# Kernel optimization log

Measured on AMD Instinct MI355X. Metric: run time of the kernel, lower is better.

The kernel has to match this reference:

```python
import jax, jax.numpy as jnp
import numpy as np

N = 1_000_000
C = 128
NBINS = 15


def setup_inputs() -> dict:
    key = jax.random.key(0)
    k1, k2 = jax.random.split(key)
    logits = jax.random.normal(k1, (N, C), dtype=jnp.float32)
    labels = jax.random.randint(k2, (N,), 0, C, dtype=jnp.int64)
    return {"logits": logits, "labels": labels}


def reference(logits, labels):
    n = logits.shape[0]
    probs = jax.nn.softmax(logits, axis=1)
    confidences = jnp.max(probs, axis=1)                      # [N]
    predictions = jnp.argmax(probs, axis=1)                   # [N]
    accuracies = (predictions == labels).astype(jnp.float32)  # [N]

    # Equal-count (adaptive) bin edges: interp(linspace(0,N,nbins+1), arange(N), sort(conf))
    sorted_conf = jnp.sort(confidences)
    q = jnp.linspace(0.0, float(n), NBINS + 1)
    edges = jnp.interp(q, jnp.arange(n, dtype=jnp.float32), sorted_conf)  # [NBINS+1]

    # Bin i covers (edges[i], edges[i+1]] to match conf.gt(lower) & conf.le(upper).
    idx = jnp.searchsorted(edges[1:-1], confidences, side="left")  # [N] in [0, NBINS-1]
    valid = (confidences > edges[0]) & (confidences <= edges[-1])
    idx = jnp.where(valid, idx, NBINS)  # dump out-of-range into extra segment

    cnt = jax.ops.segment_sum(jnp.ones_like(confidences), idx, num_segments=NBINS + 1)[:NBINS]
    csum = jax.ops.segment_sum(confidences, idx, num_segments=NBINS + 1)[:NBINS]
    asum = jax.ops.segment_sum(accuracies, idx, num_segments=NBINS + 1)[:NBINS]

    prop = cnt / jnp.float32(n)
    safe = jnp.maximum(cnt, 1.0)
    gap = jnp.abs(csum / safe - asum / safe)
    ece = jnp.sum(jnp.where(cnt > 0, gap * prop, 0.0))
    return ece.reshape(1)
```

## Files before the change

kernel.cpp:

```cpp
#include <hip/hip_runtime.h>
#include <hip/hip_bf16.h>
#include <cstdint>

#define NROWS 1000000
#define NCLS  128
#define NBINS 15

#define FBASE 0x3B000000u
#define NB    73728
#define SCAN_T 1024
#define PER   (NB / SCAN_T)

#define OFF_CONF   0u
#define OFF_ACC    4000000u
#define OFF_HIST   5000000u
#define OFF_SUB    5294912u
#define OFF_BINS   5417792u
#define OFF_DONE   5418152u
#define OFF_TGTB   5418168u
#define OFF_TGTL   5418288u
#define OFF_EDGES  5418408u
#define ZERO_BYTES (OFF_TGTB - OFF_HIST)

__device__ __forceinline__ float swz_max(float m, const int off)
{
    switch (off) {
    case 1: return fmaxf(m, __uint_as_float(__builtin_amdgcn_ds_swizzle(__float_as_uint(m), 0x041F)));
    case 2: return fmaxf(m, __uint_as_float(__builtin_amdgcn_ds_swizzle(__float_as_uint(m), 0x081F)));
    case 4: return fmaxf(m, __uint_as_float(__builtin_amdgcn_ds_swizzle(__float_as_uint(m), 0x101F)));
    default:return fmaxf(m, __uint_as_float(__builtin_amdgcn_ds_swizzle(__float_as_uint(m), 0x201F)));
    }
}
__device__ __forceinline__ float swz_add(float s, const int off)
{
    switch (off) {
    case 1: return s + __uint_as_float(__builtin_amdgcn_ds_swizzle(__float_as_uint(s), 0x041F));
    case 2: return s + __uint_as_float(__builtin_amdgcn_ds_swizzle(__float_as_uint(s), 0x081F));
    case 4: return s + __uint_as_float(__builtin_amdgcn_ds_swizzle(__float_as_uint(s), 0x101F));
    default:return s + __uint_as_float(__builtin_amdgcn_ds_swizzle(__float_as_uint(s), 0x201F));
    }
}

__global__ __launch_bounds__(256) void k_row(const float* __restrict__ logits,
                                             const int* __restrict__ labels,
                                             float* __restrict__ conf,
                                             unsigned char* __restrict__ acc,
                                             unsigned int* __restrict__ histT)
{
    const int lane = threadIdx.x & 63;
    const int wv   = threadIdx.x >> 6;
    const int g    = lane >> 4;
    const int l16  = lane & 15;
    const int wbase = blockIdx.x * 32 + wv * 8;
    const float4* lg4 = reinterpret_cast<const float4*>(logits);

#pragma unroll
    for (int half = 0; half < 2; half++) {
        const int row = wbase + half * 4 + g;
        const float4 v0 = lg4[row * 32 + l16];
        const float4 v1 = lg4[row * 32 + 16 + l16];
        const int lab = labels[row];

        float m = fmaxf(fmaxf(fmaxf(v0.x, v0.y), fmaxf(v0.z, v0.w)),
                        fmaxf(fmaxf(v1.x, v1.y), fmaxf(v1.z, v1.w)));
        m = swz_max(m, 1); m = swz_max(m, 2); m = swz_max(m, 4); m = swz_max(m, 8);

        float s = __expf(v0.x) + __expf(v0.y) + __expf(v0.z) + __expf(v0.w)
                + __expf(v1.x) + __expf(v1.y) + __expf(v1.z) + __expf(v1.w);
        s = swz_add(s, 1); s = swz_add(s, 2); s = swz_add(s, 4); s = swz_add(s, 8);

        const float c = __expf(m) / s;

        const bool hiHalf = (lab & 64) != 0;
        const float cx = hiHalf ? v1.x : v0.x;
        const float cy = hiHalf ? v1.y : v0.y;
        const float cz = hiHalf ? v1.z : v0.z;
        const float cw = hiHalf ? v1.w : v0.w;
        const int e = lab & 3;
        const float cand = (e == 0) ? cx : (e == 1) ? cy : (e == 2) ? cz : cw;
        const bool hit = (((lab >> 2) & 15) == l16) && (cand == m);
        const unsigned long long bal = __ballot(hit);

        if (l16 == 15) {
            conf[row] = c;
            acc[row]  = ((bal >> (lane & 48)) & 0xFFFFull) ? 1u : 0u;
            int ub = (int)(__float_as_uint(c) - FBASE);
            int b  = ub >> 10;
            b = b < 0 ? 0 : (b >= NB ? NB - 1 : b);
            atomicAdd(&histT[(b % PER) * 1024 + b / PER], 1u);
        }
    }
}

__device__ __forceinline__ unsigned int rank_of(int s)
{
    if (s == 0)  return 0u;
    if (s == 29) return (unsigned int)(NROWS - 1);
    int i = (s + 1) >> 1;
    unsigned int k = (unsigned int)((long long)i * NROWS / 15);
    return k + ((s & 1) ? 0u : 1u);
}

__global__ __launch_bounds__(SCAN_T) void k_scan(const unsigned int* __restrict__ histT,
                                                 int* __restrict__ tgtb,
                                                 int* __restrict__ tgtl)
{
    __shared__ unsigned int v[SCAN_T];
    const int t = threadIdx.x;
    unsigned int s = 0;
    for (int j = 0; j < PER; j++) s += histT[j * 1024 + t];
    v[t] = s;
    __syncthreads();
    for (int off = 1; off < SCAN_T; off <<= 1) {
        unsigned int x = (t >= off) ? v[t - off] : 0u;
        __syncthreads();
        v[t] += x;
        __syncthreads();
    }
    const unsigned int run0 = v[t] - s;
    for (int s2 = 0; s2 < 30; s2++) {
        unsigned int r = rank_of(s2);
        if (r >= run0 && r < run0 + s) {
            unsigned int run = run0;
            for (int j = 0; j < PER; j++) {
                unsigned int c = histT[j * 1024 + t];
                if (r < run + c) { tgtb[s2] = t * PER + j; tgtl[s2] = (int)(r - run); break; }
                run += c;
            }
        }
    }
}

__global__ __launch_bounds__(256) void k_subhist(const float* __restrict__ conf,
                                                 const int* __restrict__ tgtb,
                                                 const int* __restrict__ tgtl,
                                                 unsigned int* __restrict__ sub,
                                                 float* __restrict__ edges,
                                                 unsigned int* __restrict__ done)
{
    __shared__ int tb[30];
    if (threadIdx.x < 30) tb[threadIdx.x] = tgtb[threadIdx.x];
    __syncthreads();
    const int stride = gridDim.x * blockDim.x;
    for (int i = blockIdx.x * blockDim.x + threadIdx.x; i < NROWS / 4; i += stride) {
        float4 c4 = reinterpret_cast<const float4*>(conf)[i];
        float cv[4] = {c4.x, c4.y, c4.z, c4.w};
#pragma unroll
        for (int e = 0; e < 4; e++) {
            int ub = (int)(__float_as_uint(cv[e]) - FBASE);
            int b  = ub >> 10;
            b = b < 0 ? 0 : (b >= NB ? NB - 1 : b);
            int lo = ub & 1023;
            int match = -1;
#pragma unroll
            for (int s = 0; s < 30; s++) match = (b == tb[s]) ? s : match;
            if (match >= 0) atomicAdd(&sub[match * 1024 + lo], 1u);
        }
    }

    __syncthreads();
    __shared__ unsigned int isLast;
    if (threadIdx.x == 0) {
        __threadfence();
        isLast = (atomicAdd(done, 1u) == gridDim.x - 1) ? 1u : 0u;
    }
    __syncthreads();
    if (!isLast) return;
    __threadfence();

    __shared__ float val[32];
    const int k = threadIdx.x & 31;
    for (int slot = threadIdx.x >> 5; slot < 30; slot += 8) {
        const unsigned int local = (unsigned int)tgtl[slot];
        unsigned int cs[32];
        unsigned int csum = 0;
        const unsigned int* q = sub + slot * 1024 + k * 32;
#pragma unroll
        for (int j = 0; j < 32; j++) { cs[j] = q[j]; csum += cs[j]; }
        unsigned int incl = csum;
#pragma unroll
        for (int off = 1; off < 32; off <<= 1) {
            unsigned int x = __shfl_up(incl, off);
            if (k >= off) incl += x;
        }
        const unsigned int excl = incl - csum;
        if (local >= excl && local < excl + csum) {
            unsigned int run = excl;
            int subidx = 0;
#pragma unroll
            for (int j = 0; j < 32; j++) {
                if (local >= run && local < run + cs[j]) subidx = k * 32 + j;
                run += cs[j];
            }
            unsigned int bits = FBASE + ((unsigned int)tb[slot] << 10) + (unsigned int)subidx;
            val[slot] = __uint_as_float(bits);
        }
    }
    __syncthreads();
    if (threadIdx.x == 0) {
        edges[0]  = val[0];
        edges[15] = val[29];
        for (int i = 1; i <= 14; i++) {
            double q = (double)i * (double)NROWS / 15.0;
            long long kk = (long long)i * NROWS / 15;
            double f = q - (double)kk;
            edges[i] = (float)((1.0 - f) * (double)val[2 * i - 1] + f * (double)val[2 * i]);
        }
    }
}

__global__ __launch_bounds__(256) void k_bin(const float* __restrict__ conf,
                                             const unsigned char* __restrict__ acc,
                                             const float* __restrict__ edges,
                                             double* __restrict__ bins,
                                             unsigned int* __restrict__ done,
                                             float* __restrict__ out)
{
    __shared__ float se[16];
    __shared__ float lc[4][16], ls[4][16], la[4][16];
    const int w = threadIdx.x >> 6;
    if (threadIdx.x < 16) se[threadIdx.x] = edges[threadIdx.x];
    if (threadIdx.x < 64) {
        int a = threadIdx.x >> 4, b = threadIdx.x & 15;
        lc[a][b] = 0.f; ls[a][b] = 0.f; la[a][b] = 0.f;
    }
    __syncthreads();
    const int stride = gridDim.x * blockDim.x;
    for (int i = blockIdx.x * blockDim.x + threadIdx.x; i < NROWS / 4; i += stride) {
        float4 c4 = reinterpret_cast<const float4*>(conf)[i];
        uchar4 a4 = reinterpret_cast<const uchar4*>(acc)[i];
        float cv[4] = {c4.x, c4.y, c4.z, c4.w};
        unsigned char av[4] = {a4.x, a4.y, a4.z, a4.w};
#pragma unroll
        for (int e = 0; e < 4; e++) {
            float v = cv[e];
            if (v > se[0] && v <= se[15]) {
                int idx = 0;
#pragma unroll
                for (int j = 1; j <= 14; j++) idx += (se[j] < v) ? 1 : 0;
                atomicAdd(&lc[w][idx], 1.0f);
                atomicAdd(&ls[w][idx], v);
                atomicAdd(&la[w][idx], (float)av[e]);
            }
        }
    }
    __syncthreads();
    if (threadIdx.x < 15) {
        int t = threadIdx.x;
        atomicAdd(&bins[t],      (double)(lc[0][t] + lc[1][t] + lc[2][t] + lc[3][t]));
        atomicAdd(&bins[15 + t], (double)(ls[0][t] + ls[1][t] + ls[2][t] + ls[3][t]));
        atomicAdd(&bins[30 + t], (double)(la[0][t] + la[1][t] + la[2][t] + la[3][t]));
    }

    __syncthreads();
    __shared__ unsigned int isLast;
    if (threadIdx.x == 0) {
        __threadfence();
        isLast = (atomicAdd(done, 1u) == gridDim.x - 1) ? 1u : 0u;
    }
    __syncthreads();
    if (isLast && threadIdx.x == 0) {
        __threadfence();
        double ece = 0.0;
        for (int b = 0; b < NBINS; b++) {
            double cnt = bins[b];
            if (cnt > 0.0) {
                double safe = cnt < 1.0 ? 1.0 : cnt;
                double gap  = fabs(bins[15 + b] / safe - bins[30 + b] / safe);
                ece += gap * (cnt / (double)NROWS);
            }
        }
        out[0] = (float)ece;
    }
}

extern "C" void kernel_launch(void* const* d_in, const int* in_sizes, int n_in,
                              void* d_out, int out_size, void* d_ws, size_t ws_size,
                              hipStream_t stream)
{
    const float* logits = (const float*)d_in[0];
    const int*   labels = (const int*)d_in[1];
    char* ws = (char*)d_ws;

    float*         conf  = (float*)(ws + OFF_CONF);
    unsigned char* acc   = (unsigned char*)(ws + OFF_ACC);
    unsigned int*  histT = (unsigned int*)(ws + OFF_HIST);
    unsigned int*  sub   = (unsigned int*)(ws + OFF_SUB);
    double*        bins  = (double*)(ws + OFF_BINS);
    unsigned int*  done  = (unsigned int*)(ws + OFF_DONE);
    int*           tgtb  = (int*)(ws + OFF_TGTB);
    int*           tgtl  = (int*)(ws + OFF_TGTL);
    float*         edges = (float*)(ws + OFF_EDGES);

    hipMemsetAsync(ws + OFF_HIST, 0, ZERO_BYTES, stream);

    k_row<<<NROWS / 32, 256, 0, stream>>>(logits, labels, conf, acc, histT);
    k_scan<<<1, SCAN_T, 0, stream>>>(histT, tgtb, tgtl);
    k_subhist<<<1024, 256, 0, stream>>>(conf, tgtb, tgtl, sub, edges, done);
    k_bin<<<1024, 256, 0, stream>>>(conf, acc, edges, bins, done + 1, (float*)d_out);
}
```

Measured before the change: 257.3 us.

## Split last-block reductions into separate kernels and spread LDS atomics across slices

Replaces the last-block-done atomic pattern in the subhist and bin kernels with dedicated single-block kernels (k_edges, k_final) that read per-block partials. The bin kernel now accumulates into 64 padded LDS slices instead of 4 per-wave copies, which cuts LDS atomic contention, and writes float partials instead of doing global double atomics. The subhist kernel swaps its 30-way linear match for a 5-step binary search over the sorted target buckets, with duplicate buckets resolved in k_edges. The cost is two extra kernel launches and a larger LDS footprint per block in k_bin.

Result: faster. 215.9 us (-16.1%).

```diff
diff --git a/kernel.cpp b/kernel.cpp
--- a/kernel.cpp
+++ b/kernel.cpp
@@ -15,12 +15,11 @@
 #define OFF_ACC    4000000u
 #define OFF_HIST   5000000u
 #define OFF_SUB    5294912u
-#define OFF_BINS   5417792u
-#define OFF_DONE   5418152u
-#define OFF_TGTB   5418168u
-#define OFF_TGTL   5418288u
-#define OFF_EDGES  5418408u
-#define ZERO_BYTES (OFF_TGTB - OFF_HIST)
+#define OFF_PART   5417792u
+#define OFF_TGTB   5614400u
+#define OFF_TGTL   5614520u
+#define OFF_EDGES  5614640u
+#define ZERO_BYTES (OFF_PART - OFF_HIST)
 
 __device__ __forceinline__ float swz_max(float m, const int off)
 {
@@ -133,13 +132,10 @@
 
 __global__ __launch_bounds__(256) void k_subhist(const float* __restrict__ conf,
                                                  const int* __restrict__ tgtb,
-                                                 const int* __restrict__ tgtl,
-                                                 unsigned int* __restrict__ sub,
-                                                 float* __restrict__ edges,
-                                                 unsigned int* __restrict__ done)
-{
-    __shared__ int tb[30];
-    if (threadIdx.x < 30) tb[threadIdx.x] = tgtb[threadIdx.x];
+                                                 unsigned int* __restrict__ sub)
+{
+    __shared__ int tb[32];
+    if (threadIdx.x < 32) tb[threadIdx.x] = (threadIdx.x < 30) ? tgtb[threadIdx.x] : 0x7FFFFFFF;
     __syncthreads();
     const int stride = gridDim.x * blockDim.x;
     for (int i = blockIdx.x * blockDim.x + threadIdx.x; i < NROWS / 4; i += stride) {
@@ -150,33 +146,41 @@
             int ub = (int)(__float_as_uint(cv[e]) - FBASE);
             int b  = ub >> 10;
             b = b < 0 ? 0 : (b >= NB ? NB - 1 : b);
-            int lo = ub & 1023;
-            int match = -1;
-#pragma unroll
-            for (int s = 0; s < 30; s++) match = (b == tb[s]) ? s : match;
-            if (match >= 0) atomicAdd(&sub[match * 1024 + lo], 1u);
-        }
-    }
-
-    __syncthreads();
-    __shared__ unsigned int isLast;
-    if (threadIdx.x == 0) {
-        __threadfence();
-        isLast = (atomicAdd(done, 1u) == gridDim.x - 1) ? 1u : 0u;
-    }
-    __syncthreads();
-    if (!isLast) return;
-    __threadfence();
-
+            int lo10 = ub & 1023;
+            int lo = (tb[15] < b) ? 16 : 0;
+            lo += (tb[lo + 7] < b) ? 8 : 0;
+            lo += (tb[lo + 3] < b) ? 4 : 0;
+            lo += (tb[lo + 1] < b) ? 2 : 0;
+            lo += (tb[lo]     < b) ? 1 : 0;
+            if (tb[lo] == b) atomicAdd(&sub[lo * 1024 + lo10], 1u);
+        }
+    }
+}
+
+__global__ __launch_bounds__(1024) void k_edges(const unsigned int* __restrict__ sub,
+                        const int* __restrict__ tgtb,
+                        const int* __restrict__ tgtl,
+                        float* __restrict__ edges)
+{
     __shared__ float val[32];
+    __shared__ int tb[30], rep[30];
+    if (threadIdx.x < 30) tb[threadIdx.x] = tgtb[threadIdx.x];
+    __syncthreads();
+    if (threadIdx.x < 30) {
+        int r = 0;
+        while (tb[r] != tb[threadIdx.x]) r++;
+        rep[threadIdx.x] = r;
+    }
+    __syncthreads();
+    const int g = threadIdx.x >> 5;
     const int k = threadIdx.x & 31;
-    for (int slot = threadIdx.x >> 5; slot < 30; slot += 8) {
-        const unsigned int local = (unsigned int)tgtl[slot];
+    if (g < 30) {
+        const unsigned int local = (unsigned int)tgtl[g];
         unsigned int cs[32];
         unsigned int csum = 0;
-        const unsigned int* q = sub + slot * 1024 + k * 32;
-#pragma unroll
-        for (int j = 0; j < 32; j++) { cs[j] = q[j]; csum += cs[j]; }
+        const unsigned int* p = sub + rep[g] * 1024 + k * 32;
+#pragma unroll
+        for (int j = 0; j < 32; j++) { cs[j] = p[j]; csum += cs[j]; }
         unsigned int incl = csum;
 #pragma unroll
         for (int off = 1; off < 32; off <<= 1) {
@@ -192,8 +196,8 @@
                 if (local >= run && local < run + cs[j]) subidx = k * 32 + j;
                 run += cs[j];
             }
-            unsigned int bits = FBASE + ((unsigned int)tb[slot] << 10) + (unsigned int)subidx;
-            val[slot] = __uint_as_float(bits);
+            unsigned int bits = FBASE + ((unsigned int)tb[g] << 10) + (unsigned int)subidx;
+            val[g] = __uint_as_float(bits);
         }
     }
     __syncthreads();
@@ -212,19 +216,15 @@
 __global__ __launch_bounds__(256) void k_bin(const float* __restrict__ conf,
                                              const unsigned char* __restrict__ acc,
                                              const float* __restrict__ edges,
-                                             double* __restrict__ bins,
-                                             unsigned int* __restrict__ done,
-                                             float* __restrict__ out)
+                                             float* __restrict__ partial)
 {
     __shared__ float se[16];
-    __shared__ float lc[4][16], ls[4][16], la[4][16];
-    const int w = threadIdx.x >> 6;
+    __shared__ float sl[3][64 * 17];
     if (threadIdx.x < 16) se[threadIdx.x] = edges[threadIdx.x];
-    if (threadIdx.x < 64) {
-        int a = threadIdx.x >> 4, b = threadIdx.x & 15;
-        lc[a][b] = 0.f; ls[a][b] = 0.f; la[a][b] = 0.f;
-    }
-    __syncthreads();
+    for (int i = threadIdx.x; i < 3 * 64 * 17; i += 256) (&sl[0][0])[i] = 0.f;
+    __syncthreads();
+
+    const int slice = threadIdx.x & 63;
     const int stride = gridDim.x * blockDim.x;
     for (int i = blockIdx.x * blockDim.x + threadIdx.x; i < NROWS / 4; i += stride) {
         float4 c4 = reinterpret_cast<const float4*>(conf)[i];
@@ -238,35 +238,45 @@
                 int idx = 0;
 #pragma unroll
                 for (int j = 1; j <= 14; j++) idx += (se[j] < v) ? 1 : 0;
-                atomicAdd(&lc[w][idx], 1.0f);
-                atomicAdd(&ls[w][idx], v);
-                atomicAdd(&la[w][idx], (float)av[e]);
+                atomicAdd(&sl[0][slice * 17 + idx], 1.0f);
+                atomicAdd(&sl[1][slice * 17 + idx], v);
+                atomicAdd(&sl[2][slice * 17 + idx], (float)av[e]);
             }
         }
     }
     __syncthreads();
-    if (threadIdx.x < 15) {
-        int t = threadIdx.x;
-        atomicAdd(&bins[t],      (double)(lc[0][t] + lc[1][t] + lc[2][t] + lc[3][t]));
-        atomicAdd(&bins[15 + t], (double)(ls[0][t] + ls[1][t] + ls[2][t] + ls[3][t]));
-        atomicAdd(&bins[30 + t], (double)(la[0][t] + la[1][t] + la[2][t] + la[3][t]));
-    }
-
-    __syncthreads();
-    __shared__ unsigned int isLast;
+    if (threadIdx.x < 48) {
+        const int a = threadIdx.x >> 4, b = threadIdx.x & 15;
+        float sum = 0.f;
+        for (int s = 0; s < 64; s++) sum += sl[a][s * 17 + b];
+        partial[(a * 16 + b) * 1024 + blockIdx.x] = sum;
+    }
+}
+
+__global__ __launch_bounds__(1024) void k_final(const float* __restrict__ partial,
+                                                float* __restrict__ out)
+{
+    __shared__ double tot[48];
+    const int w    = threadIdx.x >> 6;
+    const int lane = threadIdx.x & 63;
+#pragma unroll
+    for (int c = 0; c < 3; c++) {
+        const int j = w * 3 + c;
+        double s = 0.0;
+#pragma unroll
+        for (int i = 0; i < 16; i++) s += (double)partial[j * 1024 + i * 64 + lane];
+#pragma unroll
+        for (int d = 1; d < 64; d <<= 1) s += __shfl_xor(s, d);
+        if (lane == 0) tot[j] = s;
+    }
+    __syncthreads();
     if (threadIdx.x == 0) {
-        __threadfence();
-        isLast = (atomicAdd(done, 1u) == gridDim.x - 1) ? 1u : 0u;
-    }
-    __syncthreads();
-    if (isLast && threadIdx.x == 0) {
-        __threadfence();
         double ece = 0.0;
         for (int b = 0; b < NBINS; b++) {
-            double cnt = bins[b];
+            double cnt = tot[b];
             if (cnt > 0.0) {
                 double safe = cnt < 1.0 ? 1.0 : cnt;
-                double gap  = fabs(bins[15 + b] / safe - bins[30 + b] / safe);
+                double gap  = fabs(tot[16 + b] / safe - tot[32 + b] / safe);
                 ece += gap * (cnt / (double)NROWS);
             }
         }
@@ -286,8 +296,7 @@
     unsigned char* acc   = (unsigned char*)(ws + OFF_ACC);
     unsigned int*  histT = (unsigned int*)(ws + OFF_HIST);
     unsigned int*  sub   = (unsigned int*)(ws + OFF_SUB);
-    double*        bins  = (double*)(ws + OFF_BINS);
-    unsigned int*  done  = (unsigned int*)(ws + OFF_DONE);
+    float*         part  = (float*)(ws + OFF_PART);
     int*           tgtb  = (int*)(ws + OFF_TGTB);
     int*           tgtl  = (int*)(ws + OFF_TGTL);
     float*         edges = (float*)(ws + OFF_EDGES);
@@ -296,6 +305,8 @@
 
     k_row<<<NROWS / 32, 256, 0, stream>>>(logits, labels, conf, acc, histT);
     k_scan<<<1, SCAN_T, 0, stream>>>(histT, tgtb, tgtl);
-    k_subhist<<<1024, 256, 0, stream>>>(conf, tgtb, tgtl, sub, edges, done);
-    k_bin<<<1024, 256, 0, stream>>>(conf, acc, edges, bins, done + 1, (float*)d_out);
-}
+    k_subhist<<<1024, 256, 0, stream>>>(conf, tgtb, sub);
+    k_edges<<<1, 1024, 0, stream>>>(sub, tgtb, tgtl, edges);
+    k_bin<<<1024, 256, 0, stream>>>(conf, acc, edges, part);
+    k_final<<<1, 1024, 0, stream>>>(part, (float*)d_out);
+}
```
